# Kernel optimization log

Hardware: AMD Instinct MI355X
Metric: run time of the kernel (lower is better)

Reference implementation:

```python
import jax, jax.numpy as jnp
import numpy as np

EPS = 1e-5

def _ln(x, g, b):
    mu = jnp.mean(x, axis=-1, keepdims=True)
    var = jnp.mean((x - mu) ** 2, axis=-1, keepdims=True)
    return (x - mu) * jax.lax.rsqrt(var + EPS) * g + b

def _lin(x, W, b):
    return x @ W + b

def setup_inputs() -> dict:
    B, D_IN, H = 32768, 512, 512
    key = jax.random.key(0)
    ks = jax.random.split(key, 20)
    def W(k, din, dout):
        return jax.random.normal(k, (din, dout), jnp.float32) / np.sqrt(din)
    inp = {
        'x': jax.random.normal(ks[0], (B, D_IN), jnp.float32),
        'h_prev': jax.random.normal(ks[1], (B, H), jnp.float32),
        's_prev': jax.random.normal(ks[2], (B, H), jnp.float32),
        'W_in': W(ks[3], D_IN, H), 'b_in': jnp.zeros((H,), jnp.float32),
        'g_ln_in': jnp.ones((H,), jnp.float32), 'b_ln_in': jnp.zeros((H,), jnp.float32),
        'g_ln_r': jnp.ones((H,), jnp.float32), 'b_ln_r': jnp.zeros((H,), jnp.float32),
        'g_ln_z': jnp.ones((H,), jnp.float32), 'b_ln_z': jnp.zeros((H,), jnp.float32),
        'g_ln_h': jnp.ones((H,), jnp.float32), 'b_ln_h': jnp.zeros((H,), jnp.float32),
        'W_r': W(ks[4], H, H), 'b_r': jnp.zeros((H,), jnp.float32),
        'W_z': W(ks[5], H, H), 'b_z': jnp.zeros((H,), jnp.float32),
        'W_k': W(ks[6], H, H), 'b_k': jnp.zeros((H,), jnp.float32),
        'W_v': W(ks[7], H, H), 'b_v': jnp.zeros((H,), jnp.float32),
        'W_h': W(ks[8], H, H), 'b_h': jnp.zeros((H,), jnp.float32),
        'W_d': W(ks[9], H, H), 'b_d': jnp.zeros((H,), jnp.float32),
    }
    return inp

def reference(x, h_prev, s_prev, W_in, b_in, g_ln_in, b_ln_in,
              g_ln_r, b_ln_r, g_ln_z, b_ln_z, g_ln_h, b_ln_h,
              W_r, b_r, W_z, b_z, W_k, b_k, W_v, b_v, W_h, b_h, W_d, b_d):
    # u = LN(input_proj(x))
    u = _ln(_lin(x, W_in, b_in), g_ln_in, b_ln_in)
    r = jax.nn.sigmoid(_ln(_lin(u, W_r, b_r), g_ln_r, b_ln_r))  # computed as in original (unused downstream)
    z = jax.nn.sigmoid(_ln(_lin(u, W_z, b_z), g_ln_z, b_ln_z))
    k = _lin(u, W_k, b_k)
    v = _lin(u, W_v, b_v)
    decay = jax.nn.sigmoid(_lin(u, W_d, b_d))
    s = decay * s_prev + k * v
    c = jnp.tanh(_ln(_lin(u + s, W_h, b_h), g_ln_h, b_ln_h))
    h = (1.0 - z) * c + z * h_prev
    return (h, s)
```

## Files before the change

kernel.cpp:

```cpp
#include <hip/hip_runtime.h>

typedef __attribute__((ext_vector_type(8))) short bf16x8;
typedef __attribute__((ext_vector_type(4))) float f32x4;

#define LN_EPS 1e-5f
#define MSZ ((size_t)32768 * 512)
#define WSZ ((size_t)512 * 512)

typedef const __attribute__((address_space(1))) void* gptr_t;
typedef __attribute__((address_space(3))) void* lptr_t;

__device__ __forceinline__ float b2f(unsigned short h) {
    unsigned int u = ((unsigned int)h) << 16;
    return __uint_as_float(u);
}
__device__ __forceinline__ short f2b(float f) {
    unsigned int u = __float_as_uint(f);
    unsigned int r = (u + 0x7FFFu + ((u >> 16) & 1u)) >> 16;
    return (short)(unsigned short)r;
}
__device__ __forceinline__ float sigmoid_f(float x) {
    return 1.0f / (1.0f + __expf(-x));
}
__device__ __forceinline__ float ldS(const void* p, size_t i, int isbf) {
    return isbf ? b2f(((const unsigned short*)p)[i]) : ((const float*)p)[i];
}
__device__ __forceinline__ void ld8(const void* p, size_t i, int isbf, float* o) {
    if (isbf) {
        bf16x8 v = *(const bf16x8*)((const unsigned short*)p + i);
        #pragma unroll
        for (int j = 0; j < 8; ++j) o[j] = b2f((unsigned short)v[j]);
    } else {
        f32x4 a = *(const f32x4*)((const float*)p + i);
        f32x4 b = *(const f32x4*)((const float*)p + i + 4);
        #pragma unroll
        for (int j = 0; j < 4; ++j) { o[j] = a[j]; o[4 + j] = b[j]; }
    }
}

__global__ void detect_dtype(const unsigned int* __restrict__ ones, int* __restrict__ flag) {
    if (threadIdx.x == 0 && blockIdx.x == 0)
        *flag = (ones[0] == 0x3F803F80u) ? 1 : 0;
}

__global__ __launch_bounds__(256) void transpose6(
    const void* __restrict__ s0, const void* __restrict__ s1,
    const void* __restrict__ s2, const void* __restrict__ s3,
    const void* __restrict__ s4, const void* __restrict__ s5,
    unsigned short* __restrict__ d0, unsigned short* __restrict__ d1,
    unsigned short* __restrict__ d2, unsigned short* __restrict__ d3,
    unsigned short* __restrict__ d4, unsigned short* __restrict__ d5,
    const int* __restrict__ flagp)
{
    const int isbf = *flagp;
    const void* srcs[6] = {s0, s1, s2, s3, s4, s5};
    unsigned short* dsts[6] = {d0, d1, d2, d3, d4, d5};
    const void* src = srcs[blockIdx.z];
    unsigned short* dst = dsts[blockIdx.z];

    __shared__ unsigned short tile[32][33];
    int tx = threadIdx.x, ty = threadIdx.y;
    int colbase = blockIdx.x * 32;
    int rowbase = blockIdx.y * 32;
    #pragma unroll
    for (int i = 0; i < 32; i += 8)
        tile[ty + i][tx] = (unsigned short)f2b(
            ldS(src, (size_t)(rowbase + ty + i) * 512 + colbase + tx, isbf));
    __syncthreads();
    #pragma unroll
    for (int i = 0; i < 32; i += 8)
        dst[(size_t)(colbase + ty + i) * 512 + rowbase + tx] = tile[tx][ty + i];
}

template<int OUT, bool CONV>
__global__ __launch_bounds__(512) void gemm_row(
    const void* __restrict__ Araw,
    const unsigned short* __restrict__ BT,
    const void* __restrict__ bias,
    const void* __restrict__ g0, const void* __restrict__ b0v,
    const void* __restrict__ g1, const void* __restrict__ b1v,
    const unsigned short* __restrict__ zlin,
    const void* __restrict__ h_prev,
    void* __restrict__ out,
    const int* __restrict__ flagp)
{
    const int isbf = *flagp;
    const int K = 512;
    __shared__ unsigned short smem[36864];
    unsigned short* As = smem;
    unsigned short* Bs = smem + 64 * 64;

    int t = threadIdx.x;
    int lane = t & 63;
    int wave = t >> 6;
    int wn = wave * 64;

    int b = blockIdx.x;
    int m0 = ((b & 7) * 64 + (b >> 3)) * 64;

    int lr = lane >> 3, lg = lane & 7, gsrc = lg ^ lr;
    const unsigned short* Ab = (const unsigned short*)Araw;

    size_t a_off = (size_t)(m0 + 8 * wave + lr) * K + gsrc * 8;
    size_t b_off[8];
    #pragma unroll
    for (int i = 0; i < 8; ++i)
        b_off[i] = (size_t)(64 * wave + 8 * i + lr) * K + gsrc * 8;

    int cr = t >> 3, cg = t & 7;

    int ml = lane & 15, kg = lane >> 4, sw = ml & 7;

    f32x4 acc[4][4] = {};
    const bool conv_now = CONV && !isbf;

    for (int k0 = 0; k0 < K; k0 += 64) {
        if (conv_now) {
            const float* Af = (const float*)Araw;
            size_t gi = (size_t)(m0 + cr) * K + k0 + cg * 8;
            f32x4 lo = *(const f32x4*)&Af[gi];
            f32x4 hi = *(const f32x4*)&Af[gi + 4];
            bf16x8 p;
            #pragma unroll
            for (int z = 0; z < 4; ++z) { p[z] = f2b(lo[z]); p[4 + z] = f2b(hi[z]); }
            *(bf16x8*)&As[cr * 64 + ((cg ^ (cr & 7)) * 8)] = p;
        } else {
            __builtin_amdgcn_global_load_lds(
                (gptr_t)(const void*)(Ab + a_off + k0),
                (lptr_t)(void*)(As + wave * 512), 16, 0, 0);
        }
        #pragma unroll
        for (int i = 0; i < 8; ++i)
            __builtin_amdgcn_global_load_lds(
                (gptr_t)(const void*)(BT + b_off[i] + k0),
                (lptr_t)(void*)(Bs + (wave * 8 + i) * 512), 16, 0, 0);
        __syncthreads();

        #pragma unroll
        for (int ks = 0; ks < 2; ++ks) {
            int ga = ((ks << 2) + kg) ^ sw;
            bf16x8 af[4], bfr[4];
            #pragma unroll
            for (int i = 0; i < 4; ++i)
                af[i] = *(const bf16x8*)&As[(i * 16 + ml) * 64 + ga * 8];
            #pragma unroll
            for (int j = 0; j < 4; ++j)
                bfr[j] = *(const bf16x8*)&Bs[(wn + j * 16 + ml) * 64 + ga * 8];
            #pragma unroll
            for (int i = 0; i < 4; ++i)
                #pragma unroll
                for (int j = 0; j < 4; ++j)
                    acc[i][j] = __builtin_amdgcn_mfma_f32_16x16x32_bf16(
                        af[i], bfr[j], acc[i][j], 0, 0, 0);
        }
        __syncthreads();
    }

    unsigned short* E = smem;
    int cq = lane >> 4, cl = lane & 15;
    #pragma unroll
    for (int j = 0; j < 4; ++j) {
        float bv = ldS(bias, wn + j * 16 + cl, isbf);
        #pragma unroll
        for (int i = 0; i < 4; ++i)
            #pragma unroll
            for (int r = 0; r < 4; ++r)
                E[(i * 16 + cq * 4 + r) * 520 + wn + j * 16 + cl] =
                    (unsigned short)f2b(acc[i][j][r] + bv);
    }
    __syncthreads();

    if (OUT == 0) {
        float gv[8], bv[8];
        ld8(g0, (size_t)lane * 8, isbf, gv);
        ld8(b0v, (size_t)lane * 8, isbf, bv);
        #pragma unroll
        for (int q = 0; q < 8; ++q) {
            int r = wave * 8 + q;
            bf16x8 xv = *(const bf16x8*)&E[r * 520 + lane * 8];
            float x[8], s = 0.f, s2 = 0.f;
            #pragma unroll
            for (int i = 0; i < 8; ++i) {
                x[i] = b2f((unsigned short)xv[i]);
                s += x[i]; s2 += x[i] * x[i];
            }
            #pragma unroll
            for (int off = 32; off > 0; off >>= 1) {
                s += __shfl_xor(s, off); s2 += __shfl_xor(s2, off);
            }
            float mu = s * (1.f / 512.f);
            float rs = rsqrtf(s2 * (1.f / 512.f) - mu * mu + LN_EPS);
            bf16x8 o;
            #pragma unroll
            for (int i = 0; i < 8; ++i)
                o[i] = f2b((x[i] - mu) * rs * gv[i] + bv[i]);
            *(bf16x8*)&((unsigned short*)out)[(size_t)(m0 + r) * 512 + lane * 8] = o;
        }
    } else {
        float gh[8], bh[8], gz[8], bz[8];
        ld8(g0, (size_t)lane * 8, isbf, gh);
        ld8(b0v, (size_t)lane * 8, isbf, bh);
        ld8(g1, (size_t)lane * 8, isbf, gz);
        ld8(b1v, (size_t)lane * 8, isbf, bz);
        #pragma unroll
        for (int q = 0; q < 8; ++q) {
            int r = wave * 8 + q;
            size_t base = (size_t)(m0 + r) * 512 + lane * 8;
            bf16x8 hv8 = *(const bf16x8*)&E[r * 520 + lane * 8];
            bf16x8 zv8 = *(const bf16x8*)&zlin[base];
            float hf[8], zf[8];
            float sh = 0.f, sh2 = 0.f, sz = 0.f, sz2 = 0.f;
            #pragma unroll
            for (int i = 0; i < 8; ++i) {
                hf[i] = b2f((unsigned short)hv8[i]);
                zf[i] = b2f((unsigned short)zv8[i]);
                sh += hf[i]; sh2 += hf[i] * hf[i];
                sz += zf[i]; sz2 += zf[i] * zf[i];
            }
            #pragma unroll
            for (int off = 32; off > 0; off >>= 1) {
                sh += __shfl_xor(sh, off); sh2 += __shfl_xor(sh2, off);
                sz += __shfl_xor(sz, off); sz2 += __shfl_xor(sz2, off);
            }
            float muh = sh * (1.f / 512.f);
            float rsh = rsqrtf(sh2 * (1.f / 512.f) - muh * muh + LN_EPS);
            float muz = sz * (1.f / 512.f);
            float rsz = rsqrtf(sz2 * (1.f / 512.f) - muz * muz + LN_EPS);
            float hp[8];
            ld8(h_prev, base, isbf, hp);
            float hout[8];
            #pragma unroll
            for (int i = 0; i < 8; ++i) {
                float z = sigmoid_f((zf[i] - muz) * rsz * gz[i] + bz[i]);
                float c = tanhf((hf[i] - muh) * rsh * gh[i] + bh[i]);
                hout[i] = (1.f - z) * c + z * hp[i];
            }
            if (isbf) {
                bf16x8 o;
                #pragma unroll
                for (int i = 0; i < 8; ++i) o[i] = f2b(hout[i]);
                *(bf16x8*)&((unsigned short*)out)[base] = o;
            } else {
                f32x4 lo, hi;
                #pragma unroll
                for (int i = 0; i < 4; ++i) { lo[i] = hout[i]; hi[i] = hout[4 + i]; }
                *(f32x4*)&((float*)out)[base] = lo;
                *(f32x4*)&((float*)out)[base + 4] = hi;
            }
        }
    }
}

__global__ __launch_bounds__(256) void gemm_zkvd(
    const unsigned short* __restrict__ U,
    const unsigned short* __restrict__ BT,
    const void* __restrict__ bz, const void* __restrict__ bk,
    const void* __restrict__ bv_, const void* __restrict__ bd,
    const void* __restrict__ s_prev,
    unsigned short* __restrict__ zout,
    unsigned short* __restrict__ aout,
    void* __restrict__ dout,
    const int* __restrict__ flagp)
{
    const int isbf = *flagp;
    const int K = 512;
    __shared__ unsigned short smem[20480];
    unsigned short* As = smem;

    int t = threadIdx.x;
    int lane = t & 63;
    int wave = t >> 6;
    int wm = (wave >> 1) * 32;
    int wn = (wave & 1) * 32;

    int b = blockIdx.x;
    int xcd = b & 7;
    int bi = b >> 3;
    int nb = bi & 7;
    int mi = bi >> 3;
    int m0 = (xcd * 64 + mi) * 64;
    int nc0 = nb * 64;

    int lr = lane >> 3, lg = lane & 7, gsrc = lg ^ lr;

    size_t a_off[2], b_off[8];
    #pragma unroll
    for (int i = 0; i < 2; ++i)
        a_off[i] = (size_t)(m0 + 8 * (2 * wave + i) + lr) * K + gsrc * 8;
    #pragma unroll
    for (int i = 0; i < 8; ++i)
        b_off[i] = (size_t)(wave * 512 + nc0 + 8 * i + lr) * K + gsrc * 8;

    int ml = lane & 15, kg = lane >> 4, sw = ml & 7;

    f32x4 acc[4][2][2] = {};

    for (int k0 = 0; k0 < K; k0 += 64) {
        #pragma unroll
        for (int i = 0; i < 2; ++i)
            __builtin_amdgcn_global_load_lds(
                (gptr_t)(const void*)(U + a_off[i] + k0),
                (lptr_t)(void*)(As + (2 * wave + i) * 512), 16, 0, 0);
        #pragma unroll
        for (int i = 0; i < 8; ++i)
            __builtin_amdgcn_global_load_lds(
                (gptr_t)(const void*)(BT + b_off[i] + k0),
                (lptr_t)(void*)(smem + 4096 + wave * 4096 + i * 512), 16, 0, 0);
        __syncthreads();

        #pragma unroll
        for (int ks = 0; ks < 2; ++ks) {
            int ga = ((ks << 2) + kg) ^ sw;
            bf16x8 af[2];
            #pragma unroll
            for (int i = 0; i < 2; ++i)
                af[i] = *(const bf16x8*)&As[(wm + i * 16 + ml) * 64 + ga * 8];
            #pragma unroll
            for (int s = 0; s < 4; ++s) {
                bf16x8 bf0 = *(const bf16x8*)&smem[4096 + s * 4096 + (wn + ml) * 64 + ga * 8];
                bf16x8 bf1 = *(const bf16x8*)&smem[4096 + s * 4096 + (wn + 16 + ml) * 64 + ga * 8];
                #pragma unroll
                for (int i = 0; i < 2; ++i) {
                    acc[s][i][0] = __builtin_amdgcn_mfma_f32_16x16x32_bf16(
                        af[i], bf0, acc[s][i][0], 0, 0, 0);
                    acc[s][i][1] = __builtin_amdgcn_mfma_f32_16x16x32_bf16(
                        af[i], bf1, acc[s][i][1], 0, 0, 0);
                }
            }
        }
        __syncthreads();
    }

    int cq = lane >> 4, cl = lane & 15;
    const void* biases[4] = {bz, bk, bv_, bd};
    #pragma unroll
    for (int s = 0; s < 4; ++s) {
        #pragma unroll
        for (int j = 0; j < 2; ++j) {
            float bvv = ldS(biases[s], nc0 + wn + j * 16 + cl, isbf);
            #pragma unroll
            for (int i = 0; i < 2; ++i)
                #pragma unroll
                for (int r = 0; r < 4; ++r)
                    smem[s * 4608 + (wm + i * 16 + cq * 4 + r) * 72 + wn + j * 16 + cl] =
                        (unsigned short)f2b(acc[s][i][j][r] + bvv);
        }
    }
    __syncthreads();

    int r = t >> 2;
    int c0 = (t & 3) * 16;
    #pragma unroll
    for (int g = 0; g < 2; ++g) {
        int col = c0 + g * 8;
        size_t idx = (size_t)(m0 + r) * 512 + nc0 + col;
        bf16x8 z8 = *(const bf16x8*)&smem[0 * 4608 + r * 72 + col];
        bf16x8 k8 = *(const bf16x8*)&smem[1 * 4608 + r * 72 + col];
        bf16x8 v8 = *(const bf16x8*)&smem[2 * 4608 + r * 72 + col];
        bf16x8 d8 = *(const bf16x8*)&smem[3 * 4608 + r * 72 + col];
        bf16x8 u8 = *(const bf16x8*)&U[idx];
        float sp[8];
        ld8(s_prev, idx, isbf, sp);
        float sv[8];
        bf16x8 a8;
        #pragma unroll
        for (int z = 0; z < 8; ++z) {
            float dv = sigmoid_f(b2f((unsigned short)d8[z]));
            sv[z] = dv * sp[z] + b2f((unsigned short)k8[z]) * b2f((unsigned short)v8[z]);
            a8[z] = f2b(b2f((unsigned short)u8[z]) + sv[z]);
        }
        *(bf16x8*)&zout[idx] = z8;
        *(bf16x8*)&aout[idx] = a8;
        if (isbf) {
            bf16x8 s8;
            #pragma unroll
            for (int z = 0; z < 8; ++z) s8[z] = f2b(sv[z]);
            *(bf16x8*)&((unsigned short*)dout)[MSZ + idx] = s8;
        } else {
            f32x4 lo, hi;
            #pragma unroll
            for (int z = 0; z < 4; ++z) { lo[z] = sv[z]; hi[z] = sv[4 + z]; }
            *(f32x4*)&((float*)dout)[MSZ + idx] = lo;
            *(f32x4*)&((float*)dout)[MSZ + idx + 4] = hi;
        }
    }
}

extern "C" void kernel_launch(void* const* d_in, const int* in_sizes, int n_in,
                              void* d_out, int out_size, void* d_ws, size_t ws_size,
                              hipStream_t stream)
{
    (void)in_sizes; (void)n_in; (void)out_size; (void)ws_size;

    const void* x       = d_in[0];
    const void* h_prev  = d_in[1];
    const void* s_prev  = d_in[2];
    const void* W_in    = d_in[3];
    const void* b_in    = d_in[4];
    const void* g_ln_in = d_in[5];
    const void* b_ln_in = d_in[6];
    const void* g_ln_z  = d_in[9];
    const void* b_ln_z  = d_in[10];
    const void* g_ln_h  = d_in[11];
    const void* b_ln_h  = d_in[12];
    const void* W_z     = d_in[15];
    const void* b_z     = d_in[16];
    const void* W_k     = d_in[17];
    const void* b_k     = d_in[18];
    const void* W_v     = d_in[19];
    const void* b_v     = d_in[20];
    const void* W_h     = d_in[21];
    const void* b_h     = d_in[22];
    const void* W_d     = d_in[23];
    const void* b_d     = d_in[24];

    unsigned short* ws = (unsigned short*)d_ws;
    unsigned short* U  = ws;
    unsigned short* L  = ws + MSZ;
    unsigned short* Ab = ws + 2 * MSZ;
    unsigned short* WT = ws + 3 * MSZ;
    unsigned short* WT_in = WT;
    unsigned short* WT_z  = WT + 1 * WSZ;
    unsigned short* WT_k  = WT + 2 * WSZ;
    unsigned short* WT_v  = WT + 3 * WSZ;
    unsigned short* WT_d  = WT + 4 * WSZ;
    unsigned short* WT_h  = WT + 5 * WSZ;
    int* flag = (int*)(WT + 6 * WSZ);
    (void)WT_k; (void)WT_v; (void)WT_d;

    detect_dtype<<<1, 64, 0, stream>>>((const unsigned int*)g_ln_in, flag);
    transpose6<<<dim3(16, 16, 6), dim3(32, 8), 0, stream>>>(
        W_in, W_z, W_k, W_v, W_d, W_h,
        WT_in, WT_z, WT_k, WT_v, WT_d, WT_h, flag);

    gemm_row<0, true><<<512, 512, 0, stream>>>(
        x, WT_in, b_in, g_ln_in, b_ln_in,
        nullptr, nullptr, nullptr, nullptr, U, flag);

    gemm_zkvd<<<4096, 256, 0, stream>>>(
        U, WT_z, b_z, b_k, b_v, b_d,
        s_prev, L, Ab, d_out, flag);

    gemm_row<1, false><<<512, 512, 0, stream>>>(
        Ab, WT_h, b_h, g_ln_h, b_ln_h,
        g_ln_z, b_ln_z, L, h_prev, d_out, flag);
}
```

Before: 458.0 us.

## Fuse all GEMM stages into one persistent-row megakernel keeping activations in LDS

```diff
diff --git a/kernel.cpp b/kernel.cpp
--- a/kernel.cpp
+++ b/kernel.cpp
@@ -6,9 +6,6 @@
 #define LN_EPS 1e-5f
 #define MSZ ((size_t)32768 * 512)
 #define WSZ ((size_t)512 * 512)
-
-typedef const __attribute__((address_space(1))) void* gptr_t;
-typedef __attribute__((address_space(3))) void* lptr_t;
 
 __device__ __forceinline__ float b2f(unsigned short h) {
     unsigned int u = ((unsigned int)h) << 16;
@@ -72,80 +69,79 @@
         dst[(size_t)(colbase + ty + i) * 512 + rowbase + tx] = tile[tx][ty + i];
 }
 
-template<int OUT, bool CONV>
-__global__ __launch_bounds__(512) void gemm_row(
-    const void* __restrict__ Araw,
-    const unsigned short* __restrict__ BT,
-    const void* __restrict__ bias,
-    const void* __restrict__ g0, const void* __restrict__ b0v,
-    const void* __restrict__ g1, const void* __restrict__ b1v,
-    const unsigned short* __restrict__ zlin,
+__global__ __launch_bounds__(512, 2) void lucy_mega(
+    const void* __restrict__ x,
     const void* __restrict__ h_prev,
-    void* __restrict__ out,
+    const void* __restrict__ s_prev,
+    const unsigned short* __restrict__ WT,
+    const void* __restrict__ b_in,
+    const void* __restrict__ g_ln_in, const void* __restrict__ b_ln_in,
+    const void* __restrict__ b_z, const void* __restrict__ b_k,
+    const void* __restrict__ b_v, const void* __restrict__ b_d,
+    const void* __restrict__ b_h,
+    const void* __restrict__ g_ln_z, const void* __restrict__ b_ln_z,
+    const void* __restrict__ g_ln_h, const void* __restrict__ b_ln_h,
+    unsigned short* __restrict__ Zg,
+    void* __restrict__ dout,
     const int* __restrict__ flagp)
 {
     const int isbf = *flagp;
-    const int K = 512;
-    __shared__ unsigned short smem[36864];
-    unsigned short* As = smem;
-    unsigned short* Bs = smem + 64 * 64;
+    __shared__ unsigned short A_lds[64 * 512];
 
     int t = threadIdx.x;
-    int lane = t & 63;
-    int wave = t >> 6;
+    int lane = t & 63, wave = t >> 6;
     int wn = wave * 64;
-
+    int ml = lane & 15, kq = lane >> 4, sw = ml & 7;
     int b = blockIdx.x;
     int m0 = ((b & 7) * 64 + (b >> 3)) * 64;
 
-    int lr = lane >> 3, lg = lane & 7, gsrc = lg ^ lr;
-    const unsigned short* Ab = (const unsigned short*)Araw;
-
-    size_t a_off = (size_t)(m0 + 8 * wave + lr) * K + gsrc * 8;
-    size_t b_off[8];
-    #pragma unroll
-    for (int i = 0; i < 8; ++i)
-        b_off[i] = (size_t)(64 * wave + 8 * i + lr) * K + gsrc * 8;
-
-    int cr = t >> 3, cg = t & 7;
-
-    int ml = lane & 15, kg = lane >> 4, sw = ml & 7;
-
-    f32x4 acc[4][4] = {};
-    const bool conv_now = CONV && !isbf;
-
-    for (int k0 = 0; k0 < K; k0 += 64) {
-        if (conv_now) {
-            const float* Af = (const float*)Araw;
-            size_t gi = (size_t)(m0 + cr) * K + k0 + cg * 8;
-            f32x4 lo = *(const f32x4*)&Af[gi];
-            f32x4 hi = *(const f32x4*)&Af[gi + 4];
-            bf16x8 p;
-            #pragma unroll
-            for (int z = 0; z < 4; ++z) { p[z] = f2b(lo[z]); p[4 + z] = f2b(hi[z]); }
-            *(bf16x8*)&As[cr * 64 + ((cg ^ (cr & 7)) * 8)] = p;
+    {
+        int prow = t >> 3, pg0 = t & 7;
+        if (isbf) {
+            const unsigned short* xb = (const unsigned short*)x;
+            #pragma unroll
+            for (int gi = 0; gi < 8; ++gi) {
+                int g = gi * 8 + pg0;
+                bf16x8 v = *(const bf16x8*)&xb[(size_t)(m0 + prow) * 512 + g * 8];
+                *(bf16x8*)&A_lds[prow * 512 + (g ^ (prow & 7)) * 8] = v;
+            }
         } else {
-            __builtin_amdgcn_global_load_lds(
-                (gptr_t)(const void*)(Ab + a_off + k0),
-                (lptr_t)(void*)(As + wave * 512), 16, 0, 0);
+            const float* xf = (const float*)x;
+            #pragma unroll
+            for (int gi = 0; gi < 8; ++gi) {
+                int g = gi * 8 + pg0;
+                size_t gidx = (size_t)(m0 + prow) * 512 + g * 8;
+                f32x4 lo = *(const f32x4*)&xf[gidx];
+                f32x4 hi = *(const f32x4*)&xf[gidx + 4];
+                bf16x8 p;
+                #pragma unroll
+                for (int z = 0; z < 4; ++z) { p[z] = f2b(lo[z]); p[4 + z] = f2b(hi[z]); }
+                *(bf16x8*)&A_lds[prow * 512 + (g ^ (prow & 7)) * 8] = p;
+            }
         }
-        #pragma unroll
-        for (int i = 0; i < 8; ++i)
-            __builtin_amdgcn_global_load_lds(
-                (gptr_t)(const void*)(BT + b_off[i] + k0),
-                (lptr_t)(void*)(Bs + (wave * 8 + i) * 512), 16, 0, 0);
-        __syncthreads();
-
-        #pragma unroll
-        for (int ks = 0; ks < 2; ++ks) {
-            int ga = ((ks << 2) + kg) ^ sw;
+    }
+    __syncthreads();
+
+    f32x4 acc[4][4];
+    const f32x4 zero4 = {0.f, 0.f, 0.f, 0.f};
+
+    auto GEMM = [&](const unsigned short* Bw) {
+        #pragma unroll
+        for (int i = 0; i < 4; ++i)
+            #pragma unroll
+            for (int j = 0; j < 4; ++j)
+                acc[i][j] = zero4;
+        const unsigned short* bp0 = Bw + (size_t)(wn + ml) * 512 + kq * 8;
+        #pragma unroll
+        for (int kt = 0; kt < 16; ++kt) {
+            int slot = ((kt << 2) | kq) ^ sw;
             bf16x8 af[4], bfr[4];
             #pragma unroll
             for (int i = 0; i < 4; ++i)
-                af[i] = *(const bf16x8*)&As[(i * 16 + ml) * 64 + ga * 8];
-            #pragma unroll
-            for (int j = 0; j < 4; ++j)
-                bfr[j] = *(const bf16x8*)&Bs[(wn + j * 16 + ml) * 64 + ga * 8];
+                af[i] = *(const bf16x8*)&A_lds[(i * 16 + ml) * 512 + slot * 8];
+            #pragma unroll
+            for (int j = 0; j < 4; ++j)
+                bfr[j] = *(const bf16x8*)&bp0[(size_t)j * 16 * 512 + kt * 32];
             #pragma unroll
             for (int i = 0; i < 4; ++i)
                 #pragma unroll
@@ -153,36 +149,40 @@
                     acc[i][j] = __builtin_amdgcn_mfma_f32_16x16x32_bf16(
                         af[i], bfr[j], acc[i][j], 0, 0, 0);
         }
-        __syncthreads();
-    }
-
-    unsigned short* E = smem;
-    int cq = lane >> 4, cl = lane & 15;
-    #pragma unroll
-    for (int j = 0; j < 4; ++j) {
-        float bv = ldS(bias, wn + j * 16 + cl, isbf);
-        #pragma unroll
-        for (int i = 0; i < 4; ++i)
-            #pragma unroll
-            for (int r = 0; r < 4; ++r)
-                E[(i * 16 + cq * 4 + r) * 520 + wn + j * 16 + cl] =
-                    (unsigned short)f2b(acc[i][j][r] + bv);
-    }
-    __syncthreads();
-
-    if (OUT == 0) {
-        float gv[8], bv[8];
-        ld8(g0, (size_t)lane * 8, isbf, gv);
-        ld8(b0v, (size_t)lane * 8, isbf, bv);
-        #pragma unroll
-        for (int q = 0; q < 8; ++q) {
-            int r = wave * 8 + q;
-            bf16x8 xv = *(const bf16x8*)&E[r * 520 + lane * 8];
-            float x[8], s = 0.f, s2 = 0.f;
+    };
+
+    GEMM(WT);
+    __syncthreads();
+    {
+        float bv[4];
+        #pragma unroll
+        for (int j = 0; j < 4; ++j) bv[j] = ldS(b_in, wn + j * 16 + ml, isbf);
+        #pragma unroll
+        for (int i = 0; i < 4; ++i)
+            #pragma unroll
+            for (int j = 0; j < 4; ++j)
+                #pragma unroll
+                for (int q = 0; q < 4; ++q) {
+                    int r = i * 16 + kq * 4 + q, c = wn + j * 16 + ml;
+                    A_lds[r * 512 + ((c >> 3) ^ (r & 7)) * 8 + (c & 7)] =
+                        (unsigned short)f2b(acc[i][j][q] + bv[j]);
+                }
+    }
+    __syncthreads();
+    {
+        float gv[8], bb[8];
+        ld8(g_ln_in, (size_t)lane * 8, isbf, gv);
+        ld8(b_ln_in, (size_t)lane * 8, isbf, bb);
+        #pragma unroll
+        for (int q2 = 0; q2 < 8; ++q2) {
+            int r = wave * 8 + q2;
+            int slot = lane ^ (r & 7);
+            bf16x8 xv = *(const bf16x8*)&A_lds[r * 512 + slot * 8];
+            float xx[8], s = 0.f, s2 = 0.f;
             #pragma unroll
             for (int i = 0; i < 8; ++i) {
-                x[i] = b2f((unsigned short)xv[i]);
-                s += x[i]; s2 += x[i] * x[i];
+                xx[i] = b2f((unsigned short)xv[i]);
+                s += xx[i]; s2 += xx[i] * xx[i];
             }
             #pragma unroll
             for (int off = 32; off > 0; off >>= 1) {
@@ -193,21 +193,135 @@
             bf16x8 o;
             #pragma unroll
             for (int i = 0; i < 8; ++i)
-                o[i] = f2b((x[i] - mu) * rs * gv[i] + bv[i]);
-            *(bf16x8*)&((unsigned short*)out)[(size_t)(m0 + r) * 512 + lane * 8] = o;
+                o[i] = f2b((xx[i] - mu) * rs * gv[i] + bb[i]);
+            *(bf16x8*)&A_lds[r * 512 + slot * 8] = o;
         }
-    } else {
+    }
+    __syncthreads();
+
+    GEMM(WT + WSZ);
+    {
+        float bv[4];
+        #pragma unroll
+        for (int j = 0; j < 4; ++j) bv[j] = ldS(b_z, wn + j * 16 + ml, isbf);
+        #pragma unroll
+        for (int i = 0; i < 4; ++i)
+            #pragma unroll
+            for (int j = 0; j < 4; ++j)
+                #pragma unroll
+                for (int q = 0; q < 4; ++q) {
+                    int r = i * 16 + kq * 4 + q, c = wn + j * 16 + ml;
+                    Zg[(size_t)(m0 + r) * 512 + c] =
+                        (unsigned short)f2b(acc[i][j][q] + bv[j]);
+                }
+    }
+
+    GEMM(WT + 2 * WSZ);
+    unsigned kpk[32];
+    {
+        float bv[4];
+        #pragma unroll
+        for (int j = 0; j < 4; ++j) bv[j] = ldS(b_k, wn + j * 16 + ml, isbf);
+        #pragma unroll
+        for (int i = 0; i < 4; ++i)
+            #pragma unroll
+            for (int j = 0; j < 4; ++j)
+                #pragma unroll
+                for (int q = 0; q < 4; q += 2) {
+                    unsigned lo2 = (unsigned short)f2b(acc[i][j][q] + bv[j]);
+                    unsigned hi2 = (unsigned short)f2b(acc[i][j][q + 1] + bv[j]);
+                    kpk[(i * 4 + j) * 2 + (q >> 1)] = lo2 | (hi2 << 16);
+                }
+    }
+
+    GEMM(WT + 3 * WSZ);
+    float kvf[64];
+    {
+        float bv[4];
+        #pragma unroll
+        for (int j = 0; j < 4; ++j) bv[j] = ldS(b_v, wn + j * 16 + ml, isbf);
+        #pragma unroll
+        for (int i = 0; i < 4; ++i)
+            #pragma unroll
+            for (int j = 0; j < 4; ++j)
+                #pragma unroll
+                for (int q = 0; q < 4; ++q) {
+                    int e = (i * 4 + j) * 4 + q;
+                    unsigned kp = kpk[e >> 1];
+                    float kf = b2f((unsigned short)((q & 1) ? (kp >> 16) : kp));
+                    kvf[e] = kf * b2f(f2b(acc[i][j][q] + bv[j]));
+                }
+    }
+
+    GEMM(WT + 4 * WSZ);
+    {
+        float bv[4];
+        #pragma unroll
+        for (int j = 0; j < 4; ++j) bv[j] = ldS(b_d, wn + j * 16 + ml, isbf);
+        #pragma unroll
+        for (int i = 0; i < 4; ++i)
+            #pragma unroll
+            for (int j = 0; j < 4; ++j)
+                #pragma unroll
+                for (int q = 0; q < 4; ++q) {
+                    int e = (i * 4 + j) * 4 + q;
+                    int r = i * 16 + kq * 4 + q, c = wn + j * 16 + ml;
+                    size_t idx = (size_t)(m0 + r) * 512 + c;
+                    float dv = sigmoid_f(b2f(f2b(acc[i][j][q] + bv[j])));
+                    float sp = ldS(s_prev, idx, isbf);
+                    float sv = dv * sp + kvf[e];
+                    if (isbf) ((unsigned short*)dout)[MSZ + idx] = (unsigned short)f2b(sv);
+                    else      ((float*)dout)[MSZ + idx] = sv;
+                    kvf[e] = sv;
+                }
+    }
+    __syncthreads();
+    {
+        #pragma unroll
+        for (int i = 0; i < 4; ++i)
+            #pragma unroll
+            for (int j = 0; j < 4; ++j)
+                #pragma unroll
+                for (int q = 0; q < 4; ++q) {
+                    int e = (i * 4 + j) * 4 + q;
+                    int r = i * 16 + kq * 4 + q, c = wn + j * 16 + ml;
+                    int li = r * 512 + ((c >> 3) ^ (r & 7)) * 8 + (c & 7);
+                    A_lds[li] = (unsigned short)f2b(b2f(A_lds[li]) + kvf[e]);
+                }
+    }
+    __syncthreads();
+
+    GEMM(WT + 5 * WSZ);
+    __syncthreads();
+    {
+        float bv[4];
+        #pragma unroll
+        for (int j = 0; j < 4; ++j) bv[j] = ldS(b_h, wn + j * 16 + ml, isbf);
+        #pragma unroll
+        for (int i = 0; i < 4; ++i)
+            #pragma unroll
+            for (int j = 0; j < 4; ++j)
+                #pragma unroll
+                for (int q = 0; q < 4; ++q) {
+                    int r = i * 16 + kq * 4 + q, c = wn + j * 16 + ml;
+                    A_lds[r * 512 + ((c >> 3) ^ (r & 7)) * 8 + (c & 7)] =
+                        (unsigned short)f2b(acc[i][j][q] + bv[j]);
+                }
+    }
+    __syncthreads();
+    {
         float gh[8], bh[8], gz[8], bz[8];
-        ld8(g0, (size_t)lane * 8, isbf, gh);
-        ld8(b0v, (size_t)lane * 8, isbf, bh);
-        ld8(g1, (size_t)lane * 8, isbf, gz);
-        ld8(b1v, (size_t)lane * 8, isbf, bz);
-        #pragma unroll
-        for (int q = 0; q < 8; ++q) {
-            int r = wave * 8 + q;
-            size_t base = (size_t)(m0 + r) * 512 + lane * 8;
-            bf16x8 hv8 = *(const bf16x8*)&E[r * 520 + lane * 8];
-            bf16x8 zv8 = *(const bf16x8*)&zlin[base];
+        ld8(g_ln_h, (size_t)lane * 8, isbf, gh);
+        ld8(b_ln_h, (size_t)lane * 8, isbf, bh);
+        ld8(g_ln_z, (size_t)lane * 8, isbf, gz);
+        ld8(b_ln_z, (size_t)lane * 8, isbf, bz);
+        #pragma unroll
+        for (int q2 = 0; q2 < 8; ++q2) {
+            int r = wave * 8 + q2;
+            size_t base = (size_t)(m0 + r) * 512 + (size_t)lane * 8;
+            int slot = lane ^ (r & 7);
+            bf16x8 hv8 = *(const bf16x8*)&A_lds[r * 512 + slot * 8];
+            bf16x8 zv8 = *(const bf16x8*)&Zg[base];
             float hf[8], zf[8];
             float sh = 0.f, sh2 = 0.f, sz = 0.f, sz2 = 0.f;
             #pragma unroll
@@ -232,156 +346,21 @@
             #pragma unroll
             for (int i = 0; i < 8; ++i) {
                 float z = sigmoid_f((zf[i] - muz) * rsz * gz[i] + bz[i]);
-                float c = tanhf((hf[i] - muh) * rsh * gh[i] + bh[i]);
-                hout[i] = (1.f - z) * c + z * hp[i];
+                float cc = tanhf((hf[i] - muh) * rsh * gh[i] + bh[i]);
+                hout[i] = (1.f - z) * cc + z * hp[i];
             }
             if (isbf) {
                 bf16x8 o;
                 #pragma unroll
                 for (int i = 0; i < 8; ++i) o[i] = f2b(hout[i]);
-                *(bf16x8*)&((unsigned short*)out)[base] = o;
+                *(bf16x8*)&((unsigned short*)dout)[base] = o;
             } else {
                 f32x4 lo, hi;
                 #pragma unroll
                 for (int i = 0; i < 4; ++i) { lo[i] = hout[i]; hi[i] = hout[4 + i]; }
-                *(f32x4*)&((float*)out)[base] = lo;
-                *(f32x4*)&((float*)out)[base + 4] = hi;
-            }
-        }
-    }
-}
-
-__global__ __launch_bounds__(256) void gemm_zkvd(
-    const unsigned short* __restrict__ U,
-    const unsigned short* __restrict__ BT,
-    const void* __restrict__ bz, const void* __restrict__ bk,
-    const void* __restrict__ bv_, const void* __restrict__ bd,
-    const void* __restrict__ s_prev,
-    unsigned short* __restrict__ zout,
-    unsigned short* __restrict__ aout,
-    void* __restrict__ dout,
-    const int* __restrict__ flagp)
-{
-    const int isbf = *flagp;
-    const int K = 512;
-    __shared__ unsigned short smem[20480];
-    unsigned short* As = smem;
-
-    int t = threadIdx.x;
-    int lane = t & 63;
-    int wave = t >> 6;
-    int wm = (wave >> 1) * 32;
-    int wn = (wave & 1) * 32;
-
-    int b = blockIdx.x;
-    int xcd = b & 7;
-    int bi = b >> 3;
-    int nb = bi & 7;
-    int mi = bi >> 3;
-    int m0 = (xcd * 64 + mi) * 64;
-    int nc0 = nb * 64;
-
-    int lr = lane >> 3, lg = lane & 7, gsrc = lg ^ lr;
-
-    size_t a_off[2], b_off[8];
-    #pragma unroll
-    for (int i = 0; i < 2; ++i)
-        a_off[i] = (size_t)(m0 + 8 * (2 * wave + i) + lr) * K + gsrc * 8;
-    #pragma unroll
-    for (int i = 0; i < 8; ++i)
-        b_off[i] = (size_t)(wave * 512 + nc0 + 8 * i + lr) * K + gsrc * 8;
-
-    int ml = lane & 15, kg = lane >> 4, sw = ml & 7;
-
-    f32x4 acc[4][2][2] = {};
-
-    for (int k0 = 0; k0 < K; k0 += 64) {
-        #pragma unroll
-        for (int i = 0; i < 2; ++i)
-            __builtin_amdgcn_global_load_lds(
-                (gptr_t)(const void*)(U + a_off[i] + k0),
-                (lptr_t)(void*)(As + (2 * wave + i) * 512), 16, 0, 0);
-        #pragma unroll
-        for (int i = 0; i < 8; ++i)
-            __builtin_amdgcn_global_load_lds(
-                (gptr_t)(const void*)(BT + b_off[i] + k0),
-                (lptr_t)(void*)(smem + 4096 + wave * 4096 + i * 512), 16, 0, 0);
-        __syncthreads();
-
-        #pragma unroll
-        for (int ks = 0; ks < 2; ++ks) {
-            int ga = ((ks << 2) + kg) ^ sw;
-            bf16x8 af[2];
-            #pragma unroll
-            for (int i = 0; i < 2; ++i)
-                af[i] = *(const bf16x8*)&As[(wm + i * 16 + ml) * 64 + ga * 8];
-            #pragma unroll
-            for (int s = 0; s < 4; ++s) {
-                bf16x8 bf0 = *(const bf16x8*)&smem[4096 + s * 4096 + (wn + ml) * 64 + ga * 8];
-                bf16x8 bf1 = *(const bf16x8*)&smem[4096 + s * 4096 + (wn + 16 + ml) * 64 + ga * 8];
-                #pragma unroll
-                for (int i = 0; i < 2; ++i) {
-                    acc[s][i][0] = __builtin_amdgcn_mfma_f32_16x16x32_bf16(
-                        af[i], bf0, acc[s][i][0], 0, 0, 0);
-                    acc[s][i][1] = __builtin_amdgcn_mfma_f32_16x16x32_bf16(
-                        af[i], bf1, acc[s][i][1], 0, 0, 0);
-                }
-            }
-        }
-        __syncthreads();
-    }
-
-    int cq = lane >> 4, cl = lane & 15;
-    const void* biases[4] = {bz, bk, bv_, bd};
-    #pragma unroll
-    for (int s = 0; s < 4; ++s) {
-        #pragma unroll
-        for (int j = 0; j < 2; ++j) {
-            float bvv = ldS(biases[s], nc0 + wn + j * 16 + cl, isbf);
-            #pragma unroll
-            for (int i = 0; i < 2; ++i)
-                #pragma unroll
-                for (int r = 0; r < 4; ++r)
-                    smem[s * 4608 + (wm + i * 16 + cq * 4 + r) * 72 + wn + j * 16 + cl] =
-                        (unsigned short)f2b(acc[s][i][j][r] + bvv);
-        }
-    }
-    __syncthreads();
-
-    int r = t >> 2;
-    int c0 = (t & 3) * 16;
-    #pragma unroll
-    for (int g = 0; g < 2; ++g) {
-        int col = c0 + g * 8;
-        size_t idx = (size_t)(m0 + r) * 512 + nc0 + col;
-        bf16x8 z8 = *(const bf16x8*)&smem[0 * 4608 + r * 72 + col];
-        bf16x8 k8 = *(const bf16x8*)&smem[1 * 4608 + r * 72 + col];
-        bf16x8 v8 = *(const bf16x8*)&smem[2 * 4608 + r * 72 + col];
-        bf16x8 d8 = *(const bf16x8*)&smem[3 * 4608 + r * 72 + col];
-        bf16x8 u8 = *(const bf16x8*)&U[idx];
-        float sp[8];
-        ld8(s_prev, idx, isbf, sp);
-        float sv[8];
-        bf16x8 a8;
-        #pragma unroll
-        for (int z = 0; z < 8; ++z) {
-            float dv = sigmoid_f(b2f((unsigned short)d8[z]));
-            sv[z] = dv * sp[z] + b2f((unsigned short)k8[z]) * b2f((unsigned short)v8[z]);
-            a8[z] = f2b(b2f((unsigned short)u8[z]) + sv[z]);
-        }
-        *(bf16x8*)&zout[idx] = z8;
-        *(bf16x8*)&aout[idx] = a8;
-        if (isbf) {
-            bf16x8 s8;
-            #pragma unroll
-            for (int z = 0; z < 8; ++z) s8[z] = f2b(sv[z]);
-            *(bf16x8*)&((unsigned short*)dout)[MSZ + idx] = s8;
-        } else {
-            f32x4 lo, hi;
-            #pragma unroll
-            for (int z = 0; z < 4; ++z) { lo[z] = sv[z]; hi[z] = sv[4 + z]; }
-            *(f32x4*)&((float*)dout)[MSZ + idx] = lo;
-            *(f32x4*)&((float*)dout)[MSZ + idx + 4] = hi;
+                *(f32x4*)&((float*)dout)[base] = lo;
+                *(f32x4*)&((float*)dout)[base + 4] = hi;
+            }
         }
     }
 }
@@ -415,10 +394,8 @@
     const void* b_d     = d_in[24];
 
     unsigned short* ws = (unsigned short*)d_ws;
-    unsigned short* U  = ws;
-    unsigned short* L  = ws + MSZ;
-    unsigned short* Ab = ws + 2 * MSZ;
-    unsigned short* WT = ws + 3 * MSZ;
+    unsigned short* Zg = ws;
+    unsigned short* WT = ws + MSZ;
     unsigned short* WT_in = WT;
     unsigned short* WT_z  = WT + 1 * WSZ;
     unsigned short* WT_k  = WT + 2 * WSZ;
@@ -426,22 +403,16 @@
     unsigned short* WT_d  = WT + 4 * WSZ;
     unsigned short* WT_h  = WT + 5 * WSZ;
     int* flag = (int*)(WT + 6 * WSZ);
-    (void)WT_k; (void)WT_v; (void)WT_d;
 
     detect_dtype<<<1, 64, 0, stream>>>((const unsigned int*)g_ln_in, flag);
     transpose6<<<dim3(16, 16, 6), dim3(32, 8), 0, stream>>>(
         W_in, W_z, W_k, W_v, W_d, W_h,
         WT_in, WT_z, WT_k, WT_v, WT_d, WT_h, flag);
 
-    gemm_row<0, true><<<512, 512, 0, stream>>>(
-        x, WT_in, b_in, g_ln_in, b_ln_in,
-        nullptr, nullptr, nullptr, nullptr, U, flag);
-
-    gemm_zkvd<<<4096, 256, 0, stream>>>(
-        U, WT_z, b_z, b_k, b_v, b_d,
-        s_prev, L, Ab, d_out, flag);
-
-    gemm_row<1, false><<<512, 512, 0, stream>>>(
-        Ab, WT_h, b_h, g_ln_h, b_ln_h,
-        g_ln_z, b_ln_z, L, h_prev, d_out, flag);
-}
+    lucy_mega<<<512, 512, 0, stream>>>(
+        x, h_prev, s_prev, WT,
+        b_in, g_ln_in, b_ln_in,
+        b_z, b_k, b_v, b_d, b_h,
+        g_ln_z, b_ln_z, g_ln_h, b_ln_h,
+        Zg, d_out, flag);
+}
```

Result: slower. 627.5 us (+37.0%).
